# Kernel tuning notes

Hardware: AMD Instinct MI355X
Metric: run time of the kernel (lower is better)

## Reference

```python
import jax, jax.numpy as jnp
import numpy as np

TEMPERATURE = 34.0
B, CREF, CIN, COUT, KK, KSZ, H, W = 16, 256, 256, 256, 4, 3, 56, 56
HIDDEN = int(CIN * 0.25) + 1  # 65, since ref_in_planes != 3


def setup_inputs() -> dict:
    key = jax.random.key(0)
    ks = jax.random.split(key, 7)
    ref = jax.random.normal(ks[0], (B, CREF, H, W), dtype=jnp.float32)
    x = jax.random.normal(ks[1], (B, CIN, H, W), dtype=jnp.float32)
    fc1_w = jax.random.normal(ks[2], (HIDDEN, CREF), dtype=jnp.float32) * (2.0 / CREF) ** 0.5
    fc2_w = jax.random.normal(ks[3], (KK, HIDDEN), dtype=jnp.float32) * (2.0 / HIDDEN) ** 0.5
    fc2_b = jnp.zeros((KK,), dtype=jnp.float32)
    weight = jax.random.normal(ks[4], (KK, COUT, CIN, KSZ, KSZ), dtype=jnp.float32) * 0.02
    bias = jnp.zeros((KK, COUT), dtype=jnp.float32)
    return {"ref": ref, "x": x, "fc1_w": fc1_w, "fc2_w": fc2_w,
            "fc2_b": fc2_b, "weight": weight, "bias": bias}


def _attention(ref, fc1_w, fc2_w, fc2_b):
    pooled = jnp.mean(ref, axis=(2, 3))                 # [B, CREF] adaptive avgpool to 1x1
    h = jax.nn.relu(pooled @ fc1_w.T)                   # [B, HIDDEN] (1x1 conv == matmul)
    logits = h @ fc2_w.T + fc2_b                        # [B, K]
    return jax.nn.softmax(logits / TEMPERATURE, axis=-1)


def _conv_one(xi, wi):
    # xi: [CIN, H, W], wi: [COUT, CIN, k, k]; stride 1, padding 1, dilation 1, groups 1
    out = jax.lax.conv_general_dilated(
        xi[None], wi, window_strides=(1, 1), padding=((1, 1), (1, 1)),
        dimension_numbers=("NCHW", "OIHW", "NCHW"))
    return out[0]


def reference(ref, x, fc1_w, fc2_w, fc2_b, weight, bias):
    attn = _attention(ref, fc1_w, fc2_w, fc2_b)                  # [B, K]
    agg_w = jnp.einsum("bk,koihw->boihw", attn, weight)          # per-sample kernels
    agg_b = attn @ bias                                          # [B, COUT]
    out = jax.vmap(_conv_one)(x, agg_w)                          # [B, COUT, H, W]
    return out + agg_b[:, :, None, None]
```

## Files before the change

### kernel.cpp

```cpp
#include <hip/hip_runtime.h>
#include <hip/hip_bf16.h>

#define BB    16
#define CREF  256
#define CINC  256
#define COUTC 256
#define KKN   4
#define HH    56
#define WWW   56
#define HIDDEN 65
#define NPIX  3136
#define PPIX  3364
#define TEMP  34.0f

typedef __bf16 bf16x8 __attribute__((ext_vector_type(8)));
typedef float  f32x4  __attribute__((ext_vector_type(4)));

#define WS_ATTN   0
#define WS_AGGB   4096
#define WS_POOL   24576
#define WS_AGGW   65536
#define WS_XPAD   19005440

#define ABUF  73728
#define XB_SZ 24576

__global__ void pool_k(const float* __restrict__ ref, float* __restrict__ pooled,
                       __bf16* __restrict__ xpad) {
    int wid = threadIdx.x >> 6, lane = threadIdx.x & 63;
    int gw = blockIdx.x * 4 + wid;
    const float4* r4 = reinterpret_cast<const float4*>(ref) + (size_t)gw * 784;
    float s = 0.f;
    for (int i = lane; i < 784; i += 64) {
        float4 v = r4[i];
        s += v.x + v.y + v.z + v.w;
    }
    for (int o = 32; o; o >>= 1) s += __shfl_xor(s, o);
    if (lane == 0) pooled[gw] = s * (1.0f / (float)NPIX);

    if (gw < 3648) {
        int b = gw / 228, i = gw % 228;
        int ph, pw;
        if (i < 58)       { ph = 0;        pw = i; }
        else if (i < 116) { ph = 57;       pw = i - 58; }
        else if (i < 172) { ph = i - 115;  pw = 0; }
        else              { ph = i - 171;  pw = 57; }
        uint2* dst = (uint2*)(xpad + ((size_t)b * PPIX + ph * 58 + pw) * 256);
        dst[lane] = (uint2){0u, 0u};
    }
}

__global__ void attn_k(const float* __restrict__ pooled, const float* __restrict__ fc1w,
                       const float* __restrict__ fc2w, const float* __restrict__ fc2b,
                       const float* __restrict__ bias,
                       float* __restrict__ attn, float* __restrict__ aggb) {
    int b = blockIdx.x;
    int t = threadIdx.x;
    __shared__ float sh[HIDDEN + 7];
    __shared__ float sl[KKN];
    __shared__ float sa[KKN];
    const float* prow = pooled + b * CREF;
    {
        int j = t >> 2, sub = t & 3;
        const float4* w4 = (const float4*)(fc1w + j * CREF + sub * 64);
        const float4* p4 = (const float4*)(prow + sub * 64);
        float s = 0.f;
#pragma unroll
        for (int k = 0; k < 16; ++k) {
            float4 w = w4[k], p = p4[k];
            s += w.x * p.x + w.y * p.y + w.z * p.z + w.w * p.w;
        }
        s += __shfl_xor(s, 1); s += __shfl_xor(s, 2);
        if (sub == 0) sh[j] = fmaxf(s, 0.f);
    }
    if (t < 4) {
        const float4* w4 = (const float4*)(fc1w + 64 * CREF + t * 64);
        const float4* p4 = (const float4*)(prow + t * 64);
        float s = 0.f;
#pragma unroll
        for (int k = 0; k < 16; ++k) {
            float4 w = w4[k], p = p4[k];
            s += w.x * p.x + w.y * p.y + w.z * p.z + w.w * p.w;
        }
        s += __shfl_xor(s, 1); s += __shfl_xor(s, 2);
        if (t == 0) sh[64] = fmaxf(s, 0.f);
    }
    __syncthreads();
    if (t < KKN) {
        float s = fc2b[t];
        for (int j = 0; j < HIDDEN; ++j) s += sh[j] * fc2w[t * HIDDEN + j];
        sl[t] = s * (1.0f / TEMP);
    }
    __syncthreads();
    if (t == 0) {
        float m = fmaxf(fmaxf(sl[0], sl[1]), fmaxf(sl[2], sl[3]));
        float e0 = expf(sl[0] - m), e1 = expf(sl[1] - m);
        float e2 = expf(sl[2] - m), e3 = expf(sl[3] - m);
        float inv = 1.f / (e0 + e1 + e2 + e3);
        sa[0] = e0 * inv; sa[1] = e1 * inv; sa[2] = e2 * inv; sa[3] = e3 * inv;
        attn[b * 4 + 0] = sa[0]; attn[b * 4 + 1] = sa[1];
        attn[b * 4 + 2] = sa[2]; attn[b * 4 + 3] = sa[3];
    }
    __syncthreads();
    {
        float s = 0.f;
#pragma unroll
        for (int k = 0; k < KKN; ++k) s += sa[k] * bias[k * COUTC + t];
        aggb[b * COUTC + t] = s;
    }
}

__global__ void aggw_k(const float* __restrict__ attn, const float* __restrict__ weight,
                       __bf16* __restrict__ aggw) {
    __shared__ float s_attn[64];
    int t = threadIdx.x;
    int co = t >> 5, cr = t & 31;
    int cout = blockIdx.x * 8 + co;
    int cb8 = blockIdx.y;
    int cin = cb8 * 32 + cr;
    if (t < 64) s_attn[t] = attn[t];
    __syncthreads();
    float w[4][9];
#pragma unroll
    for (int k = 0; k < 4; ++k) {
        const float* wp = weight + ((size_t)(k * 256 + cout) * 256 + cin) * 9;
#pragma unroll
        for (int tp = 0; tp < 9; ++tp) w[k][tp] = wp[tp];
    }
    int ch = cout >> 7, coutl = cout & 127;
    int cing = cr >> 3, cinr = cr & 7;
    for (int b = 0; b < BB; ++b) {
        float a0 = s_attn[b * 4 + 0], a1 = s_attn[b * 4 + 1];
        float a2 = s_attn[b * 4 + 2], a3 = s_attn[b * 4 + 3];
#pragma unroll
        for (int tap = 0; tap < 9; ++tap) {
            float v = a0 * w[0][tap] + a1 * w[1][tap] + a2 * w[2][tap] + a3 * w[3][tap];
            size_t e = (size_t)((b * 2 + ch) * 8 + cb8) * 36864 +
                       (tap * 4 + cing) * 1024 + coutl * 8 + cinr;
            aggw[e] = (__bf16)v;
        }
    }
}

__global__ void xpad_int_k(const float* __restrict__ x, __bf16* __restrict__ xpad) {
    __shared__ float tile[64][65];
    int pt = blockIdx.x;
    int cg = blockIdx.y;
    int b  = blockIdx.z;
    int q = threadIdx.x >> 6, l = threadIdx.x & 63;
    for (int k = 0; k < 16; ++k) {
        int cl = q * 16 + k;
        tile[cl][l] = x[((size_t)(b * 256 + cg * 64 + cl)) * NPIX + pt * 64 + l];
    }
    __syncthreads();
    for (int k = 0; k < 16; ++k) {
        int pl = q * 16 + k;
        int pixel = pt * 64 + pl;
        int h = pixel / 56, w = pixel - h * 56;
        xpad[(((size_t)b * PPIX + (h + 1) * 58 + (w + 1)) * 256) + cg * 64 + l] =
            (__bf16)tile[l][pl];
    }
}

__global__ __launch_bounds__(256) void conv_k(const __bf16* __restrict__ xpad,
                                              const __bf16* __restrict__ aggw,
                                              const float* __restrict__ aggb,
                                              float* __restrict__ out) {
    __shared__ __attribute__((aligned(16))) char xs[2 * XB_SZ + 1024];

    const int orig = blockIdx.x;
    const int logical = (orig & 7) * 56 + (orig >> 3);
    const int b  = logical / 28;
    const int r  = logical - b * 28;
    const int rp = r >> 1;
    const int ch = r & 1;
    const int tid = threadIdx.x;
    const int wid = tid >> 6, lane = tid & 63;
    const int l15 = lane & 15, l4 = lane >> 4;
    const int h0 = rp * 4;

    const char* xb  = (const char*)xpad + (size_t)b * PPIX * 512;
    const char* awb = (const char*)aggw + (size_t)((b * 2 + ch) * 8) * ABUF;
    const int voff = l4 * 2048 + l15 * 16;

    f32x4 acc[8][4];
#pragma unroll
    for (int m = 0; m < 8; ++m)
#pragma unroll
        for (int n = 0; n < 4; ++n) acc[m][n] = (f32x4){0.f, 0.f, 0.f, 0.f};

    bf16x8 af[2][8];
    bf16x8 bfr[2][4];

    auto XSTAGE = [&](int buf, int c) {
#pragma unroll
        for (int j = 0; j < 6; ++j) {
            const char* src = xb + (size_t)((h0 + j) * 58 + lane) * 512 + c * 64 + wid * 16;
            __builtin_amdgcn_global_load_lds(
                (const __attribute__((address_space(1))) void*)src,
                (__attribute__((address_space(3))) void*)(xs + buf * XB_SZ + (wid * 6 + j) * 1024),
                16, 0, 0);
        }
    };

#define ALOAD(P, C, T) do { \
    const char* ap_ = awb + (size_t)(C) * ABUF + (T) * 8192 + voff; \
    _Pragma("unroll") \
    for (int m_ = 0; m_ < 8; ++m_) af[P][m_] = *(const bf16x8*)(ap_ + m_ * 256); \
} while (0)

#define BLOAD(P, T, LB) do { \
    const int kh_ = (T) / 3, kw_ = (T) - kh_ * 3; \
    _Pragma("unroll") \
    for (int nf_ = 0; nf_ < 4; ++nf_) \
        bfr[P][nf_] = *(const bf16x8*)((LB) + \
            (((l4 * 6 + wid + kh_) * 64) + nf_ * 16 + l15 + kw_) * 16); \
} while (0)

    XSTAGE(0, 0);
    ALOAD(0, 0, 0);
    __syncthreads();

    int cur = 0;
    for (int c = 0; c < 8; ++c) {
        if (c < 7) XSTAGE(cur ^ 1, c + 1);
        const char* lb = xs + cur * XB_SZ;
        BLOAD(0, 0, lb);
#pragma unroll
        for (int t = 0; t < 9; ++t) {
            const int p = t & 1, q = p ^ 1;
            if (t < 8) {
                ALOAD(q, c, t + 1);
                BLOAD(q, t + 1, lb);
            } else if (c < 7) {
                ALOAD(q, c + 1, 0);
            }
            __builtin_amdgcn_s_setprio(1);
#pragma unroll
            for (int nf = 0; nf < 4; ++nf)
#pragma unroll
                for (int m = 0; m < 8; ++m)
                    acc[m][nf] = __builtin_amdgcn_mfma_f32_16x16x32_bf16(
                        af[p][m], bfr[p][nf], acc[m][nf], 0, 0, 0);
            __builtin_amdgcn_s_setprio(0);
        }
        if (c < 7) {
#pragma unroll
            for (int m = 0; m < 8; ++m) af[0][m] = af[1][m];
        }
        __syncthreads();
        cur ^= 1;
    }
#undef ALOAD
#undef BLOAD

    const int row = rp * 4 + wid;
#pragma unroll
    for (int m = 0; m < 8; ++m) {
#pragma unroll
        for (int i = 0; i < 4; ++i) {
            int cout = ch * 128 + m * 16 + l4 * 4 + i;
            float bv = aggb[b * COUTC + cout];
            float* op = out + ((size_t)(b * COUTC + cout) * NPIX + row * 56);
#pragma unroll
            for (int nf = 0; nf < 3; ++nf)
                __builtin_nontemporal_store(acc[m][nf][i] + bv, op + nf * 16 + l15);
            if (l15 < 8)
                __builtin_nontemporal_store(acc[m][3][i] + bv, op + 48 + l15);
        }
    }
}

extern "C" void kernel_launch(void* const* d_in, const int* in_sizes, int n_in,
                              void* d_out, int out_size, void* d_ws, size_t ws_size,
                              hipStream_t stream) {
    (void)in_sizes; (void)n_in; (void)out_size; (void)ws_size;
    const float* ref    = (const float*)d_in[0];
    const float* x      = (const float*)d_in[1];
    const float* fc1w   = (const float*)d_in[2];
    const float* fc2w   = (const float*)d_in[3];
    const float* fc2b   = (const float*)d_in[4];
    const float* weight = (const float*)d_in[5];
    const float* bias   = (const float*)d_in[6];
    float* out = (float*)d_out;
    char* ws = (char*)d_ws;

    float*  attn   = (float*)(ws + WS_ATTN);
    float*  aggb   = (float*)(ws + WS_AGGB);
    float*  pooled = (float*)(ws + WS_POOL);
    __bf16* aggw   = (__bf16*)(ws + WS_AGGW);
    __bf16* xpad   = (__bf16*)(ws + WS_XPAD);

    pool_k<<<1024, 256, 0, stream>>>(ref, pooled, xpad);
    attn_k<<<16, 256, 0, stream>>>(pooled, fc1w, fc2w, fc2b, bias, attn, aggb);
    aggw_k<<<dim3(32, 8), 256, 0, stream>>>(attn, weight, aggw);
    xpad_int_k<<<dim3(49, 4, 16), 256, 0, stream>>>(x, xpad);
    conv_k<<<448, 256, 0, stream>>>(xpad, aggw, aggb, out);
}
```

Before: 118.4 us.

## Stage conv weight fragments through LDS with a 4-slot async pipeline

The conv kernel now stages the per-tap weight (A) fragments into a 4-slot LDS ring using async global-to-LDS loads issued three taps ahead. Previously each wave read them directly from global memory into registers. The single per-channel-block __syncthreads is replaced by per-tap vmcnt waits plus barriers, and the next x tile is prefetched mid-iteration. This is meant to hide global load latency behind the MFMAs. In exchange it adds a barrier after every tap, uses more dynamic LDS (about 80KB), and requests two blocks per CU via launch bounds, which may raise register pressure.

```diff
diff --git a/kernel.cpp b/kernel.cpp
--- a/kernel.cpp
+++ b/kernel.cpp
@@ -24,6 +24,8 @@
 
 #define ABUF  73728
 #define XB_SZ 24576
+#define ASLOT 8192
+#define LDS_TOT (2*XB_SZ + 4*ASLOT)
 
 __global__ void pool_k(const float* __restrict__ ref, float* __restrict__ pooled,
                        __bf16* __restrict__ xpad) {
@@ -162,11 +164,13 @@
     }
 }
 
-__global__ __launch_bounds__(256) void conv_k(const __bf16* __restrict__ xpad,
-                                              const __bf16* __restrict__ aggw,
-                                              const float* __restrict__ aggb,
-                                              float* __restrict__ out) {
-    __shared__ __attribute__((aligned(16))) char xs[2 * XB_SZ + 1024];
+__global__ __launch_bounds__(256, 2) void conv_k(const __bf16* __restrict__ xpad,
+                                                 const __bf16* __restrict__ aggw,
+                                                 const float* __restrict__ aggb,
+                                                 float* __restrict__ out) {
+    extern __shared__ __attribute__((aligned(16))) char smem[];
+    char* xs = smem;
+    char* as = smem + 2 * XB_SZ;
 
     const int orig = blockIdx.x;
     const int logical = (orig & 7) * 56 + (orig >> 3);
@@ -181,7 +185,6 @@
 
     const char* xb  = (const char*)xpad + (size_t)b * PPIX * 512;
     const char* awb = (const char*)aggw + (size_t)((b * 2 + ch) * 8) * ABUF;
-    const int voff = l4 * 2048 + l15 * 16;
 
     f32x4 acc[8][4];
 #pragma unroll
@@ -202,14 +205,25 @@
                 16, 0, 0);
         }
     };
-
-#define ALOAD(P, C, T) do { \
-    const char* ap_ = awb + (size_t)(C) * ABUF + (T) * 8192 + voff; \
+    auto ASTAGE = [&](int slot, int c, int tap) {
+#pragma unroll
+        for (int j = 0; j < 2; ++j) {
+            int k = wid * 2 + j;
+            const char* src = awb + (size_t)c * ABUF + tap * 8192 + k * 1024 + lane * 16;
+            __builtin_amdgcn_global_load_lds(
+                (const __attribute__((address_space(1))) void*)src,
+                (__attribute__((address_space(3))) void*)(as + slot * ASLOT + k * 1024),
+                16, 0, 0);
+        }
+    };
+
+#define ALOADF(P, SLOT) do { \
+    const char* ap_ = as + (SLOT) * ASLOT + l4 * 2048 + l15 * 16; \
     _Pragma("unroll") \
     for (int m_ = 0; m_ < 8; ++m_) af[P][m_] = *(const bf16x8*)(ap_ + m_ * 256); \
 } while (0)
 
-#define BLOAD(P, T, LB) do { \
+#define BLOADF(P, T, LB) do { \
     const int kh_ = (T) / 3, kw_ = (T) - kh_ * 3; \
     _Pragma("unroll") \
     for (int nf_ = 0; nf_ < 4; ++nf_) \
@@ -217,42 +231,70 @@
             (((l4 * 6 + wid + kh_) * 64) + nf_ * 16 + l15 + kw_) * 16); \
 } while (0)
 
+#define MFMAS(P) do { \
+    __builtin_amdgcn_s_setprio(1); \
+    _Pragma("unroll") \
+    for (int nf_ = 0; nf_ < 4; ++nf_) \
+        _Pragma("unroll") \
+        for (int m_ = 0; m_ < 8; ++m_) \
+            acc[m_][nf_] = __builtin_amdgcn_mfma_f32_16x16x32_bf16( \
+                af[P][m_], bfr[P][nf_], acc[m_][nf_], 0, 0, 0); \
+    __builtin_amdgcn_s_setprio(0); \
+} while (0)
+
+#define SUBBAR(N) do { \
+        asm volatile("s_waitcnt vmcnt(" #N ")" ::: "memory"); \
+        __builtin_amdgcn_s_barrier(); \
+        __builtin_amdgcn_sched_barrier(0); } while (0)
+
     XSTAGE(0, 0);
-    ALOAD(0, 0, 0);
-    __syncthreads();
+    ASTAGE(0, 0, 0);
+    ASTAGE(1, 0, 1);
+    ASTAGE(2, 0, 2);
+    SUBBAR(0);
+    ALOADF(0, 0);
+    BLOADF(0, 0, xs);
 
     int cur = 0;
     for (int c = 0; c < 8; ++c) {
-        if (c < 7) XSTAGE(cur ^ 1, c + 1);
-        const char* lb = xs + cur * XB_SZ;
-        BLOAD(0, 0, lb);
+        const int cs = c & 3;
+        const char* lb  = xs + cur * XB_SZ;
+        const char* lbn = xs + (cur ^ 1) * XB_SZ;
 #pragma unroll
         for (int t = 0; t < 9; ++t) {
             const int p = t & 1, q = p ^ 1;
+            if (t < 6) {
+                ASTAGE((t + cs + 3) & 3, c, t + 3);
+            } else if (c < 7) {
+                ASTAGE((t + cs + 3) & 3, c + 1, t - 6);
+            }
+            if (t == 5 && c < 7) XSTAGE(cur ^ 1, c + 1);
             if (t < 8) {
-                ALOAD(q, c, t + 1);
-                BLOAD(q, t + 1, lb);
+                ALOADF(q, (t + 1 + cs) & 3);
+                BLOADF(q, t + 1, lb);
             } else if (c < 7) {
-                ALOAD(q, c + 1, 0);
+                ALOADF(q, (cs + 1) & 3);
+                BLOADF(q, 0, lbn);
             }
-            __builtin_amdgcn_s_setprio(1);
-#pragma unroll
-            for (int nf = 0; nf < 4; ++nf)
-#pragma unroll
-                for (int m = 0; m < 8; ++m)
-                    acc[m][nf] = __builtin_amdgcn_mfma_f32_16x16x32_bf16(
-                        af[p][m], bfr[p][nf], acc[m][nf], 0, 0, 0);
-            __builtin_amdgcn_s_setprio(0);
+            MFMAS(p);
+            if (t <= 4)      { SUBBAR(2); }
+            else if (t == 5) { if (c < 7) SUBBAR(8); else SUBBAR(2); }
+            else if (t == 6) { if (c < 7) SUBBAR(8); else SUBBAR(0); }
+            else if (t == 7) { if (c < 7) SUBBAR(2); else SUBBAR(0); }
+            else             { if (c < 7) SUBBAR(2);  }
         }
         if (c < 7) {
 #pragma unroll
             for (int m = 0; m < 8; ++m) af[0][m] = af[1][m];
-        }
-        __syncthreads();
+#pragma unroll
+            for (int n = 0; n < 4; ++n) bfr[0][n] = bfr[1][n];
+        }
         cur ^= 1;
     }
-#undef ALOAD
-#undef BLOAD
+#undef ALOADF
+#undef BLOADF
+#undef MFMAS
+#undef SUBBAR
 
     const int row = rp * 4 + wid;
 #pragma unroll
@@ -291,9 +333,12 @@
     __bf16* aggw   = (__bf16*)(ws + WS_AGGW);
     __bf16* xpad   = (__bf16*)(ws + WS_XPAD);
 
+    hipFuncSetAttribute((const void*)conv_k,
+                        hipFuncAttributeMaxDynamicSharedMemorySize, LDS_TOT);
+
     pool_k<<<1024, 256, 0, stream>>>(ref, pooled, xpad);
     attn_k<<<16, 256, 0, stream>>>(pooled, fc1w, fc2w, fc2b, bias, attn, aggb);
     aggw_k<<<dim3(32, 8), 256, 0, stream>>>(attn, weight, aggw);
     xpad_int_k<<<dim3(49, 4, 16), 256, 0, stream>>>(x, xpad);
-    conv_k<<<448, 256, 0, stream>>>(xpad, aggw, aggb, out);
-}
+    conv_k<<<448, 256, LDS_TOT, stream>>>(xpad, aggw, aggb, out);
+}
```

Result: faster. 103.0 us (-13.0%).
